# Kernel optimization log

Hardware: AMD Instinct MI355X
Metric: run time of the kernel (lower is better)

The kernel has to match this reference:

```python
import jax, jax.numpy as jnp
import numpy as np

B, S, H, R = 64, 2048, 512, 256
NEG = -1.0e9


def setup_inputs() -> dict:
    key = jax.random.key(0)
    ks = jax.random.split(key, 12)
    sc_h = 1.0 / np.sqrt(H)
    sc_r = 1.0 / np.sqrt(R)
    return {
        "sent_h": jax.random.normal(ks[0], (B, S, H), jnp.float32),
        "rel": jax.random.normal(ks[1], (B, R), jnp.float32),
        "pool": jax.random.normal(ks[2], (B, H), jnp.float32),
        "mask": jax.random.randint(ks[3], (B, S), 0, 2, jnp.int32),
        "Wg_w": jax.random.normal(ks[4], (H, H), jnp.float32) * sc_h,
        "Wg_b": jnp.zeros((H,), jnp.float32),
        "Wh_w": jax.random.normal(ks[5], (H, H), jnp.float32) * sc_h,
        "Wh_b": jnp.zeros((H,), jnp.float32),
        "Wr_w": jax.random.normal(ks[6], (H, R), jnp.float32) * sc_r,
        "Wr_b": jnp.zeros((H,), jnp.float32),
        "alpha_w": jax.random.normal(ks[7], (1, H), jnp.float32) * sc_h,
        "alpha_b": jnp.zeros((1,), jnp.float32),
    }


def reference(sent_h, rel, pool, mask, Wg_w, Wg_b, Wh_w, Wh_b, Wr_w, Wr_b, alpha_w, alpha_b):
    # linear projections (torch Linear: x @ W.T + b)
    relation = rel @ Wr_w.T + Wr_b          # [B, H]
    sent = jnp.einsum('bsh,kh->bsk', sent_h, Wh_w) + Wh_b  # [B, S, H]
    global_sen = pool @ Wg_w.T + Wg_b       # [B, H]
    mix = jnp.tanh(relation[:, None, :] + sent + global_sen[:, None, :])  # [B, S, H]
    weight = jnp.einsum('bsh,h->bs', mix, alpha_w[0]) + alpha_b[0]        # [B, S]
    weight = jnp.where(mask == 0, NEG, weight)
    weight_ = jax.nn.softmax(weight, axis=-1)
    att_res = jnp.einsum('bs,bsh->bh', weight_, sent)  # [B, H]
    return (att_res, weight_)
```

## Files before the change

kernel.cpp:

```cpp
#include <hip/hip_runtime.h>
#include <cstdint>
#include <cstddef>

#define B_ 64
#define S_ 2048
#define H_ 512
#define R_ 256
#define M_ (B_ * S_)
#define NEGV (-1.0e9f)

typedef short short8 __attribute__((ext_vector_type(8)));
typedef unsigned short u16x8 __attribute__((ext_vector_type(8)));
typedef float f32x4 __attribute__((ext_vector_type(4)));
typedef unsigned short u16;

__device__ __forceinline__ u16 f2b(float x) {
    union { float f; uint32_t u; } c; c.f = x;
    uint32_t u = c.u;
    uint32_t r = (u + 0x7fffu + ((u >> 16) & 1u)) >> 16;
    return (u16)r;
}
__device__ __forceinline__ float b2f(u16 u) {
    union { uint32_t u; float f; } c; c.u = ((uint32_t)u) << 16;
    return c.f;
}
__device__ __forceinline__ uint32_t pk2(float lo, float hi) {
    uint32_t r;
    asm("v_cvt_pk_bf16_f32 %0, %1, %2" : "=v"(r) : "v"(lo), "v"(hi));
    return r;
}
__device__ __forceinline__ void load_lds16(const void* g, void* l) {
    __builtin_amdgcn_global_load_lds((__attribute__((address_space(1))) void*)g,
                                     (__attribute__((address_space(3))) void*)l,
                                     16, 0, 0);
}

__global__ void k_base(const float* __restrict__ rel, const float* __restrict__ pool,
                       const float* __restrict__ Wg_w, const float* __restrict__ Wg_b,
                       const float* __restrict__ Wh_b,
                       const float* __restrict__ Wr_w, const float* __restrict__ Wr_b,
                       const float* __restrict__ whw, float* __restrict__ base,
                       u16* __restrict__ whwb) {
    int tid = threadIdx.x;
    {
        int gi = blockIdx.x * 256 + tid;
        float4 v = ((const float4*)whw)[gi];
        ushort4 o; o.x = f2b(v.x); o.y = f2b(v.y); o.z = f2b(v.z); o.w = f2b(v.w);
        ((ushort4*)whwb)[gi] = o;
    }
    int b = blockIdx.x >> 2, q = blockIdx.x & 3;
    __shared__ __attribute__((aligned(16))) float srel[R_];
    __shared__ __attribute__((aligned(16))) float spool[H_];
    __shared__ float accs[128];
    srel[tid & 255] = rel[b * R_ + (tid & 255)];
    for (int i = tid; i < H_; i += 256) spool[i] = pool[b * H_ + i];
    __syncthreads();
    int kk = tid & 127, half = tid >> 7;
    int k = q * 128 + kk;
    float acc = 0.f;
    if (half == 0) {
        acc = Wr_b[k] + Wg_b[k] + Wh_b[k];
        const float4* wr = (const float4*)(Wr_w + (size_t)k * R_);
        #pragma unroll 8
        for (int r4 = 0; r4 < R_ / 4; ++r4) {
            float4 w = wr[r4]; float4 x = ((const float4*)srel)[r4];
            acc += w.x * x.x + w.y * x.y + w.z * x.z + w.w * x.w;
        }
        const float4* wg = (const float4*)(Wg_w + (size_t)k * H_);
        #pragma unroll 8
        for (int h4 = 0; h4 < 32; ++h4) {
            float4 w = wg[h4]; float4 x = ((const float4*)spool)[h4];
            acc += w.x * x.x + w.y * x.y + w.z * x.z + w.w * x.w;
        }
    } else {
        const float4* wg = (const float4*)(Wg_w + (size_t)k * H_);
        #pragma unroll 8
        for (int h4 = 32; h4 < 128; ++h4) {
            float4 w = wg[h4]; float4 x = ((const float4*)spool)[h4];
            acc += w.x * x.x + w.y * x.y + w.z * x.z + w.w * x.w;
        }
    }
    if (half) accs[kk] = acc;
    __syncthreads();
    if (!half) base[b * H_ + k] = acc + accs[kk];
}

__launch_bounds__(256, 4)
__global__ void k_gemm(const float* __restrict__ A32,
                       const u16* __restrict__ Bw,
                       const float* __restrict__ base,
                       const float* __restrict__ alpha,
                       float* __restrict__ partial)
{
    const int K = 512;
    const int NT = 16;
    int j = blockIdx.x;
    int xcd  = j & 7;
    int slot = j >> 3;
    int nb   = slot & 3;
    int mb   = (slot >> 2) * 8 + xcd;
    int m0 = mb * 128;
    int n0 = nb * 128;
    int b  = m0 >> 11;

    int tid = threadIdx.x;
    int w  = tid >> 6;
    int l  = tid & 63;
    int wm = w & 1, wn = w >> 1;
    int lr = l & 15;
    int lq = l >> 4;

    __shared__ __attribute__((aligned(16))) u16 smA[2][128 * 32];
    __shared__ __attribute__((aligned(16))) u16 smB[2][128 * 32];
    __shared__ float red[2][2][64];

    f32x4 zero = {0.f, 0.f, 0.f, 0.f};
    f32x4 acc[4][4];
    #pragma unroll
    for (int i = 0; i < 4; ++i)
        #pragma unroll
        for (int jj = 0; jj < 4; ++jj) acc[i][jj] = zero;

    int arow[2];
    #pragma unroll
    for (int i = 0; i < 2; ++i) arow[i] = (w * 2 + i) * 16 + lr;

    float4 av[2][2];

    auto LOAD_A = [&](int kt) {
        int k0 = kt * 32;
        #pragma unroll
        for (int i = 0; i < 2; ++i) {
            const float4* ga = (const float4*)(A32 + (size_t)(m0 + arow[i]) * K + k0 + lq * 8);
            av[i][0] = ga[0];
            av[i][1] = ga[1];
        }
    };
    auto WRITE_A = [&](int buf) {
        #pragma unroll
        for (int i = 0; i < 2; ++i) {
            uint4 pv;
            pv.x = pk2(av[i][0].x, av[i][0].y);
            pv.y = pk2(av[i][0].z, av[i][0].w);
            pv.z = pk2(av[i][1].x, av[i][1].y);
            pv.w = pk2(av[i][1].z, av[i][1].w);
            *(uint4*)(smA[buf] + (w * 2 + i) * 512 + l * 8) = pv;
        }
    };
    auto STAGE_B = [&](int buf, int kt) {
        int k0 = kt * 32;
        #pragma unroll
        for (int i = 0; i < 2; ++i) {
            int c = w * 2 + i;
            const u16* gb = Bw + (size_t)(n0 + c * 16 + lr) * K + k0 + lq * 8;
            load_lds16(gb, smB[buf] + c * 512);
        }
    };

    LOAD_A(0);
    STAGE_B(0, 0);
    WRITE_A(0);
    __syncthreads();

    #pragma unroll
    for (int kt = 0; kt < NT; ++kt) {
        int cur = kt & 1;
        if (kt < NT - 1) {
            LOAD_A(kt + 1);
            STAGE_B(cur ^ 1, kt + 1);
        }
        __builtin_amdgcn_s_setprio(1);
        {
            short8 af[4], bf[4];
            #pragma unroll
            for (int mi = 0; mi < 4; ++mi)
                af[mi] = *(const short8*)(smA[cur] + (wm * 4 + mi) * 512 + l * 8);
            #pragma unroll
            for (int ni = 0; ni < 4; ++ni)
                bf[ni] = *(const short8*)(smB[cur] + (wn * 4 + ni) * 512 + l * 8);
            #pragma unroll
            for (int mi = 0; mi < 4; ++mi)
                #pragma unroll
                for (int ni = 0; ni < 4; ++ni)
                    acc[mi][ni] = __builtin_amdgcn_mfma_f32_16x16x32_bf16(af[mi], bf[ni], acc[mi][ni], 0, 0, 0);
        }
        __builtin_amdgcn_s_setprio(0);
        if (kt < NT - 1) WRITE_A(cur ^ 1);
        __syncthreads();
    }

    const float C2 = 2.8853900817779268f;
    float base2[4], a2[4];
    float asum = 0.f;
    #pragma unroll
    for (int ni = 0; ni < 4; ++ni) {
        int n = n0 + wn * 64 + ni * 16 + lr;
        base2[ni] = C2 * base[b * H_ + n];
        float al  = alpha[n];
        a2[ni] = 2.0f * al;
        asum  += al;
    }
    #pragma unroll
    for (int mi = 0; mi < 4; ++mi) {
        #pragma unroll
        for (int r = 0; r < 4; ++r) {
            float s = asum;
            #pragma unroll
            for (int ni = 0; ni < 4; ++ni) {
                float f  = fmaf(acc[mi][ni][r], C2, base2[ni]);
                float e  = __builtin_amdgcn_exp2f(f);
                float rr = __builtin_amdgcn_rcpf(e + 1.0f);
                s = fmaf(-a2[ni], rr, s);
            }
            s += __shfl_xor(s, 1);
            s += __shfl_xor(s, 2);
            s += __shfl_xor(s, 4);
            s += __shfl_xor(s, 8);
            if (lr == 0) red[wm][wn][mi * 16 + lq * 4 + r] = s;
        }
    }
    __syncthreads();
    if (tid < 128) {
        int wmi = tid >> 6, row = tid & 63;
        float sum = red[wmi][0][row] + red[wmi][1][row];
        partial[(size_t)nb * M_ + m0 + wmi * 64 + row] = sum;
    }
}

__global__ void k_softmax(const float* __restrict__ partial, const int* __restrict__ mask,
                          const float* __restrict__ alpha_b, float* __restrict__ wout) {
    int b = blockIdx.x;
    int tid = threadIdx.x;
    __shared__ float sred[8];
    float x[8];
    float ab = alpha_b[0];
    float lmax = -3.0e38f;
    #pragma unroll
    for (int jj = 0; jj < 8; ++jj) {
        int s = tid + jj * 256;
        size_t m = (size_t)b * S_ + s;
        float v = partial[m] + partial[(size_t)M_ + m] + partial[2 * (size_t)M_ + m] + partial[3 * (size_t)M_ + m] + ab;
        if (mask[b * S_ + s] == 0) v = NEGV;
        x[jj] = v;
        lmax = fmaxf(lmax, v);
    }
    #pragma unroll
    for (int off = 1; off < 64; off <<= 1) lmax = fmaxf(lmax, __shfl_xor(lmax, off));
    int wv = tid >> 6, l = tid & 63;
    if (l == 0) sred[wv] = lmax;
    __syncthreads();
    float gmax = fmaxf(fmaxf(sred[0], sred[1]), fmaxf(sred[2], sred[3]));
    float lsum = 0.f;
    #pragma unroll
    for (int jj = 0; jj < 8; ++jj) { x[jj] = __expf(x[jj] - gmax); lsum += x[jj]; }
    #pragma unroll
    for (int off = 1; off < 64; off <<= 1) lsum += __shfl_xor(lsum, off);
    if (l == 0) sred[4 + wv] = lsum;
    __syncthreads();
    float inv = 1.f / (sred[4] + sred[5] + sred[6] + sred[7]);
    #pragma unroll
    for (int jj = 0; jj < 8; ++jj) {
        int s = tid + jj * 256;
        wout[(size_t)b * S_ + s] = x[jj] * inv;
    }
}

__global__ void k_wsum(const float* __restrict__ sent, const float* __restrict__ wrow_g,
                       float* __restrict__ tpart) {
    int b  = blockIdx.x >> 4;
    int ss = blockIdx.x & 15;
    int tid = threadIdx.x;
    __shared__ float wrow[128];
    if (tid < 128) wrow[tid] = wrow_g[(size_t)b * S_ + ss * 128 + tid];
    __syncthreads();
    const float* bp = sent + ((size_t)b * S_ + (size_t)ss * 128) * H_ + tid * 2;
    float ax = 0.f, ay = 0.f;
    for (int r0 = 0; r0 < 128; r0 += 8) {
        float2 v[8];
        #pragma unroll
        for (int u = 0; u < 8; ++u)
            v[u] = *(const float2*)(bp + (size_t)(r0 + u) * H_);
        #pragma unroll
        for (int u = 0; u < 8; ++u) {
            float wgt = wrow[r0 + u];
            ax = fmaf(wgt, v[u].x, ax);
            ay = fmaf(wgt, v[u].y, ay);
        }
    }
    float* tp = tpart + ((size_t)ss * B_ + b) * H_ + tid * 2;
    tp[0] = ax; tp[1] = ay;
}

__global__ void k_att(const float* __restrict__ tpart, const float* __restrict__ Whw,
                      const float* __restrict__ Whb, float* __restrict__ out) {
    int tid = threadIdx.x;
    int b = blockIdx.x >> 2, q = blockIdx.x & 3;
    __shared__ __attribute__((aligned(16))) float st[H_];
    __shared__ float accs[128];
    for (int i = tid; i < H_; i += 256) {
        float s = 0.f;
        #pragma unroll
        for (int ss = 0; ss < 16; ++ss)
            s += tpart[((size_t)ss * B_ + b) * H_ + i];
        st[i] = s;
    }
    __syncthreads();
    int hh = tid & 127, half = tid >> 7;
    int h = q * 128 + hh;
    const float4* wr = (const float4*)(Whw + (size_t)h * H_) + half * 64;
    const float4* sx = (const float4*)st + half * 64;
    float acc = 0.f;
    #pragma unroll 8
    for (int i = 0; i < 64; ++i) {
        float4 w = wr[i]; float4 x = sx[i];
        acc += w.x * x.x + w.y * x.y + w.z * x.z + w.w * x.w;
    }
    if (half) accs[hh] = acc;
    __syncthreads();
    if (!half) out[(size_t)b * H_ + h] = acc + accs[hh] + Whb[h];
}

extern "C" void kernel_launch(void* const* d_in, const int* in_sizes, int n_in,
                              void* d_out, int out_size, void* d_ws, size_t ws_size,
                              hipStream_t stream) {
    const float* sent_h  = (const float*)d_in[0];
    const float* rel     = (const float*)d_in[1];
    const float* pool    = (const float*)d_in[2];
    const int*   mask    = (const int*)d_in[3];
    const float* Wg_w    = (const float*)d_in[4];
    const float* Wg_b    = (const float*)d_in[5];
    const float* Wh_w    = (const float*)d_in[6];
    const float* Wh_b    = (const float*)d_in[7];
    const float* Wr_w    = (const float*)d_in[8];
    const float* Wr_b    = (const float*)d_in[9];
    const float* alpha_w = (const float*)d_in[10];
    const float* alpha_b = (const float*)d_in[11];
    float* out = (float*)d_out;

    char* ws = (char*)d_ws;
    u16*   whwb    = (u16*)ws;
    float* base    = (float*)(ws + 524288);
    float* partial = (float*)(ws + 524288 + 131072);
    float* tpart   = (float*)(ws + 524288 + 131072 + 2097152);

    float* att_out = out;
    float* w_out   = out + B_ * H_;

    k_base<<<dim3(256), dim3(256), 0, stream>>>(rel, pool, Wg_w, Wg_b, Wh_b, Wr_w, Wr_b, Wh_w, base, whwb);
    k_gemm<<<dim3((M_ / 128) * 4), dim3(256), 0, stream>>>(sent_h, whwb, base, alpha_w, partial);
    k_softmax<<<dim3(B_), dim3(256), 0, stream>>>(partial, mask, alpha_b, w_out);
    k_wsum<<<dim3(B_ * 16), dim3(256), 0, stream>>>(sent_h, w_out, tpart);
    k_att<<<dim3(256), dim3(256), 0, stream>>>(tpart, Wh_w, Wh_b, att_out);
}
```

Measured before the change: 547.0 us.

## Stage fp32 A tiles directly to LDS with triple-buffered async pipeline

The fp32 A operand is now copied global-to-LDS asynchronously with global_load_lds instead of going through registers, and is converted to bf16 when fragments are read from LDS. The LDS buffers become three-deep, so loads run two k-tiles ahead, and waiting uses explicit vmcnt counts plus raw barriers instead of __syncthreads. This is meant to hide global load latency and free VGPRs. In exchange A in LDS doubles in size (fp32) across three stages, which lowers occupancy, and every wave now repeats the bf16 conversion work when it reads A.

```diff
diff --git a/kernel.cpp b/kernel.cpp
--- a/kernel.cpp
+++ b/kernel.cpp
@@ -13,6 +13,8 @@
 typedef unsigned short u16x8 __attribute__((ext_vector_type(8)));
 typedef float f32x4 __attribute__((ext_vector_type(4)));
 typedef unsigned short u16;
+
+#define VMCNT(N)  asm volatile("s_waitcnt vmcnt(" #N ")" ::: "memory")
 
 __device__ __forceinline__ u16 f2b(float x) {
     union { float f; uint32_t u; } c; c.f = x;
@@ -85,7 +87,7 @@
     if (!half) base[b * H_ + k] = acc + accs[kk];
 }
 
-__launch_bounds__(256, 4)
+__launch_bounds__(256)
 __global__ void k_gemm(const float* __restrict__ A32,
                        const u16* __restrict__ Bw,
                        const float* __restrict__ base,
@@ -110,8 +112,8 @@
     int lr = l & 15;
     int lq = l >> 4;
 
-    __shared__ __attribute__((aligned(16))) u16 smA[2][128 * 32];
-    __shared__ __attribute__((aligned(16))) u16 smB[2][128 * 32];
+    __shared__ __attribute__((aligned(16))) float smA[3][8 * 512];
+    __shared__ __attribute__((aligned(16))) u16   smB[3][8 * 512];
     __shared__ float red[2][2][64];
 
     f32x4 zero = {0.f, 0.f, 0.f, 0.f};
@@ -121,63 +123,49 @@
         #pragma unroll
         for (int jj = 0; jj < 4; ++jj) acc[i][jj] = zero;
 
-    int arow[2];
-    #pragma unroll
-    for (int i = 0; i < 2; ++i) arow[i] = (w * 2 + i) * 16 + lr;
-
-    float4 av[2][2];
-
-    auto LOAD_A = [&](int kt) {
-        int k0 = kt * 32;
-        #pragma unroll
-        for (int i = 0; i < 2; ++i) {
-            const float4* ga = (const float4*)(A32 + (size_t)(m0 + arow[i]) * K + k0 + lq * 8);
-            av[i][0] = ga[0];
-            av[i][1] = ga[1];
-        }
-    };
-    auto WRITE_A = [&](int buf) {
-        #pragma unroll
-        for (int i = 0; i < 2; ++i) {
-            uint4 pv;
-            pv.x = pk2(av[i][0].x, av[i][0].y);
-            pv.y = pk2(av[i][0].z, av[i][0].w);
-            pv.z = pk2(av[i][1].x, av[i][1].y);
-            pv.w = pk2(av[i][1].z, av[i][1].w);
-            *(uint4*)(smA[buf] + (w * 2 + i) * 512 + l * 8) = pv;
-        }
-    };
-    auto STAGE_B = [&](int buf, int kt) {
+    auto STAGE = [&](int buf, int kt) {
         int k0 = kt * 32;
         #pragma unroll
         for (int i = 0; i < 2; ++i) {
             int c = w * 2 + i;
+            #pragma unroll
+            for (int h = 0; h < 2; ++h) {
+                const float* ga = A32 + (size_t)(m0 + c * 16 + lr) * K + k0 + lq * 8 + h * 4;
+                load_lds16(ga, &smA[buf][c * 512 + h * 256]);
+            }
             const u16* gb = Bw + (size_t)(n0 + c * 16 + lr) * K + k0 + lq * 8;
-            load_lds16(gb, smB[buf] + c * 512);
+            load_lds16(gb, &smB[buf][c * 512]);
         }
     };
 
-    LOAD_A(0);
-    STAGE_B(0, 0);
-    WRITE_A(0);
-    __syncthreads();
+    STAGE(0, 0);
+    STAGE(1, 1);
+    VMCNT(6);
+    __builtin_amdgcn_s_barrier();
+    __builtin_amdgcn_sched_barrier(0);
 
     #pragma unroll
     for (int kt = 0; kt < NT; ++kt) {
-        int cur = kt & 1;
-        if (kt < NT - 1) {
-            LOAD_A(kt + 1);
-            STAGE_B(cur ^ 1, kt + 1);
-        }
+        const int cur = kt % 3;
+        if (kt < NT - 2) STAGE((kt + 2) % 3, kt + 2);
         __builtin_amdgcn_s_setprio(1);
         {
             short8 af[4], bf[4];
             #pragma unroll
-            for (int mi = 0; mi < 4; ++mi)
-                af[mi] = *(const short8*)(smA[cur] + (wm * 4 + mi) * 512 + l * 8);
+            for (int mi = 0; mi < 4; ++mi) {
+                const float* ca = &smA[cur][(wm * 4 + mi) * 512];
+                f32x4 lo = *(const f32x4*)(ca + l * 4);
+                f32x4 hi = *(const f32x4*)(ca + 256 + l * 4);
+                uint32_t d0 = pk2(lo[0], lo[1]);
+                uint32_t d1 = pk2(lo[2], lo[3]);
+                uint32_t d2 = pk2(hi[0], hi[1]);
+                uint32_t d3 = pk2(hi[2], hi[3]);
+                uint4 uv = make_uint4(d0, d1, d2, d3);
+                af[mi] = *(short8*)&uv;
+            }
             #pragma unroll
             for (int ni = 0; ni < 4; ++ni)
-                bf[ni] = *(const short8*)(smB[cur] + (wn * 4 + ni) * 512 + l * 8);
+                bf[ni] = *(const short8*)(&smB[cur][(wn * 4 + ni) * 512] + l * 8);
             #pragma unroll
             for (int mi = 0; mi < 4; ++mi)
                 #pragma unroll
@@ -185,8 +173,11 @@
                     acc[mi][ni] = __builtin_amdgcn_mfma_f32_16x16x32_bf16(af[mi], bf[ni], acc[mi][ni], 0, 0, 0);
         }
         __builtin_amdgcn_s_setprio(0);
-        if (kt < NT - 1) WRITE_A(cur ^ 1);
-        __syncthreads();
+        if (kt < NT - 1) {
+            if (kt < NT - 2) { VMCNT(6); } else { VMCNT(0); }
+            __builtin_amdgcn_s_barrier();
+            __builtin_amdgcn_sched_barrier(0);
+        }
     }
 
     const float C2 = 2.8853900817779268f;
```

Measured after the change: 598.1 us. +9.3%, slower.

## Fuse softmax, weighted sum and output projection into one tail kernel

Applied to the files above, without the earlier changes.

Merges the softmax, weighted-sum and Wh projection kernels into a single kernel with 512 blocks. Each block recomputes the full softmax for its batch row, reduces a 256-row slice of sent_h, projects the partial sum through Wh_w, and atomically adds the result into the output, which is zeroed with a memset beforehand. This removes two launches and the tpart workspace round trip. In exchange, the softmax is computed redundantly eight times per row, each block reads the whole 1 MB Wh_w matrix (much more Wh traffic than before), and float atomics make the summation order nondeterministic.

```diff
diff --git a/kernel.cpp b/kernel.cpp
--- a/kernel.cpp
+++ b/kernel.cpp
@@ -19,10 +19,6 @@
     uint32_t u = c.u;
     uint32_t r = (u + 0x7fffu + ((u >> 16) & 1u)) >> 16;
     return (u16)r;
-}
-__device__ __forceinline__ float b2f(u16 u) {
-    union { uint32_t u; float f; } c; c.u = ((uint32_t)u) << 16;
-    return c.f;
 }
 __device__ __forceinline__ uint32_t pk2(float lo, float hi) {
     uint32_t r;
@@ -227,11 +223,16 @@
     }
 }
 
-__global__ void k_softmax(const float* __restrict__ partial, const int* __restrict__ mask,
-                          const float* __restrict__ alpha_b, float* __restrict__ wout) {
-    int b = blockIdx.x;
+__global__ void k_tail(const float* __restrict__ partial, const int* __restrict__ mask,
+                       const float* __restrict__ alpha_b, const float* __restrict__ sent,
+                       const float* __restrict__ Whw, const float* __restrict__ Whb,
+                       float* __restrict__ wout, float* __restrict__ att_out) {
+    int b  = blockIdx.x >> 3;
+    int sl = blockIdx.x & 7;
     int tid = threadIdx.x;
     __shared__ float sred[8];
+    __shared__ float sw[256];
+    __shared__ __attribute__((aligned(16))) float st[H_];
     float x[8];
     float ab = alpha_b[0];
     float lmax = -3.0e38f;
@@ -260,64 +261,42 @@
     float inv = 1.f / (sred[4] + sred[5] + sred[6] + sred[7]);
     #pragma unroll
     for (int jj = 0; jj < 8; ++jj) {
-        int s = tid + jj * 256;
-        wout[(size_t)b * S_ + s] = x[jj] * inv;
-    }
-}
-
-__global__ void k_wsum(const float* __restrict__ sent, const float* __restrict__ wrow_g,
-                       float* __restrict__ tpart) {
-    int b  = blockIdx.x >> 4;
-    int ss = blockIdx.x & 15;
-    int tid = threadIdx.x;
-    __shared__ float wrow[128];
-    if (tid < 128) wrow[tid] = wrow_g[(size_t)b * S_ + ss * 128 + tid];
-    __syncthreads();
-    const float* bp = sent + ((size_t)b * S_ + (size_t)ss * 128) * H_ + tid * 2;
+        float wvv = x[jj] * inv;
+        if (sl == 0) wout[(size_t)b * S_ + tid + jj * 256] = wvv;
+        if (jj == sl) sw[tid] = wvv;
+    }
+    __syncthreads();
+
+    const float* bp = sent + ((size_t)b * S_ + (size_t)sl * 256) * H_ + tid * 2;
     float ax = 0.f, ay = 0.f;
-    for (int r0 = 0; r0 < 128; r0 += 8) {
+    for (int r0 = 0; r0 < 256; r0 += 8) {
         float2 v[8];
         #pragma unroll
         for (int u = 0; u < 8; ++u)
             v[u] = *(const float2*)(bp + (size_t)(r0 + u) * H_);
         #pragma unroll
         for (int u = 0; u < 8; ++u) {
-            float wgt = wrow[r0 + u];
+            float wgt = sw[r0 + u];
             ax = fmaf(wgt, v[u].x, ax);
             ay = fmaf(wgt, v[u].y, ay);
         }
     }
-    float* tp = tpart + ((size_t)ss * B_ + b) * H_ + tid * 2;
-    tp[0] = ax; tp[1] = ay;
-}
-
-__global__ void k_att(const float* __restrict__ tpart, const float* __restrict__ Whw,
-                      const float* __restrict__ Whb, float* __restrict__ out) {
-    int tid = threadIdx.x;
-    int b = blockIdx.x >> 2, q = blockIdx.x & 3;
-    __shared__ __attribute__((aligned(16))) float st[H_];
-    __shared__ float accs[128];
-    for (int i = tid; i < H_; i += 256) {
-        float s = 0.f;
-        #pragma unroll
-        for (int ss = 0; ss < 16; ++ss)
-            s += tpart[((size_t)ss * B_ + b) * H_ + i];
-        st[i] = s;
-    }
-    __syncthreads();
-    int hh = tid & 127, half = tid >> 7;
-    int h = q * 128 + hh;
-    const float4* wr = (const float4*)(Whw + (size_t)h * H_) + half * 64;
-    const float4* sx = (const float4*)st + half * 64;
-    float acc = 0.f;
-    #pragma unroll 8
-    for (int i = 0; i < 64; ++i) {
-        float4 w = wr[i]; float4 x = sx[i];
-        acc += w.x * x.x + w.y * x.y + w.z * x.z + w.w * x.w;
-    }
-    if (half) accs[hh] = acc;
-    __syncthreads();
-    if (!half) out[(size_t)b * H_ + h] = acc + accs[hh] + Whb[h];
+    st[tid * 2]     = ax;
+    st[tid * 2 + 1] = ay;
+    __syncthreads();
+
+    #pragma unroll
+    for (int rep = 0; rep < 2; ++rep) {
+        int h = tid + rep * 256;
+        const float4* wr = (const float4*)(Whw + (size_t)h * H_);
+        float acc = (sl == 0) ? Whb[h] : 0.f;
+        #pragma unroll 8
+        for (int i = 0; i < 128; ++i) {
+            float4 wv2 = wr[i]; float4 xv = ((const float4*)st)[i];
+            acc += wv2.x * xv.x + wv2.y * xv.y + wv2.z * xv.z + wv2.w * xv.w;
+        }
+        atomicAdd(att_out + (size_t)b * H_ + h, acc);
+    }
 }
 
 extern "C" void kernel_launch(void* const* d_in, const int* in_sizes, int n_in,
@@ -341,14 +320,12 @@
     u16*   whwb    = (u16*)ws;
     float* base    = (float*)(ws + 524288);
     float* partial = (float*)(ws + 524288 + 131072);
-    float* tpart   = (float*)(ws + 524288 + 131072 + 2097152);
 
     float* att_out = out;
     float* w_out   = out + B_ * H_;
 
+    hipMemsetAsync(att_out, 0, (size_t)B_ * H_ * sizeof(float), stream);
     k_base<<<dim3(256), dim3(256), 0, stream>>>(rel, pool, Wg_w, Wg_b, Wh_b, Wr_w, Wr_b, Wh_w, base, whwb);
     k_gemm<<<dim3((M_ / 128) * 4), dim3(256), 0, stream>>>(sent_h, whwb, base, alpha_w, partial);
-    k_softmax<<<dim3(B_), dim3(256), 0, stream>>>(partial, mask, alpha_b, w_out);
-    k_wsum<<<dim3(B_ * 16), dim3(256), 0, stream>>>(sent_h, w_out, tpart);
-    k_att<<<dim3(256), dim3(256), 0, stream>>>(tpart, Wh_w, Wh_b, att_out);
-}
+    k_tail<<<dim3(B_ * 8), dim3(256), 0, stream>>>(partial, mask, alpha_b, sent_h, Wh_w, Wh_b, w_out, att_out);
+}
```

Result: slower. 587.6 us (+7.4%).
